# Performance work log

Measured on AMD Instinct MI355X. Metric: run time of the kernel, lower is better.

Reference implementation:

```python
import jax, jax.numpy as jnp
import numpy as np

N, E = 50000, 800000
IN_F, OUT_F, EMB, KER = 64, 64, 3, 4


def setup_inputs() -> dict:
    key = jax.random.key(0)
    ks = jax.random.split(key, 6)
    x = jax.random.normal(ks[0], (N, IN_F), dtype=jnp.float32)
    edge_idx = jax.random.randint(ks[1], (2, E), 0, N, dtype=jnp.int64)
    spec_domain = jax.random.normal(ks[2], (N, EMB), dtype=jnp.float32)
    weight = 0.1 * jax.random.normal(ks[3], (IN_F, OUT_F, KER), dtype=jnp.float32)
    bias_p = 0.1 * jax.random.normal(ks[4], (OUT_F,), dtype=jnp.float32)
    mu = 0.005 * jax.random.normal(ks[5], (EMB, KER), dtype=jnp.float32)
    sig = jnp.ones((1, KER), dtype=jnp.float32)  # repo default 60140 underflows exp with random embeddings
    return {"x": x, "edge_idx": edge_idx, "spec_domain": spec_domain,
            "weight": weight, "bias_p": bias_p, "mu": mu, "sig": sig}


def reference(x, edge_idx, spec_domain, weight, bias_p, mu, sig):
    n = x.shape[0]
    row, col = edge_idx[0], edge_idx[1]
    # support for all kernels at once: [N, out, K]
    support = jnp.einsum('ni,iok->nok', x, weight)
    # per-edge Gaussian kernel values: [E, K]
    diff = spec_domain[row] - spec_domain[col]               # [E, emb]
    dm = diff[:, :, None] - mu[None, :, :]                   # [E, emb, K]
    qq = -0.5 * jnp.sum(dm * dm, axis=1)                     # [E, K]
    value = jnp.exp(sig[0][None, :] * qq)                    # [E, K]
    # sparse mm: out[row] += value * support[col], per kernel
    msgs = value[:, None, :] * support[col]                  # [E, out, K]
    out = jax.ops.segment_sum(msgs, row, num_segments=n)     # [N, out, K]
    return out.sum(axis=2) + bias_p
```

## Files before the change

### kernel.cpp

```cpp
#include <hip/hip_runtime.h>
#include <hip/hip_fp16.h>

#define FIN 64
#define CAP 64
#define CSTR 16

__global__ __launch_bounds__(256) void prep_kernel(const int* __restrict__ eidx,
                                                   int* __restrict__ flag,
                                                   int4* __restrict__ cnt4, int n4) {
    int i = blockIdx.x * blockDim.x + threadIdx.x;
    if (i == 0) {
        int nz = 0;
        for (int j = 1; j < 16; j += 2) nz |= eidx[j];
        *flag = (nz == 0) ? 1 : 0;
    }
    int4 z = make_int4(0, 0, 0, 0);
    for (int t = i; t < n4; t += gridDim.x * blockDim.x) cnt4[t] = z;
}

__global__ __launch_bounds__(256) void mid_kernel(const float* __restrict__ x,
                                                  const float* __restrict__ weight,
                                                  __half* __restrict__ sup,
                                                  const int* __restrict__ eidx,
                                                  const int* __restrict__ flag,
                                                  int* __restrict__ cnt,
                                                  int* __restrict__ scol,
                                                  int n, int e_total) {
    const int t = threadIdx.x;

    __shared__ float xs[32][64];
    const int rowbase = blockIdx.x * 32;

    if (rowbase < n) {
        {
            const float4* __restrict__ x4 = (const float4*)(x + (size_t)rowbase * 64);
            float4* __restrict__ s4 = (float4*)&xs[0][0];
            int limit = (n - rowbase) * 16;
            if (limit > 512) limit = 512;
            #pragma unroll
            for (int j = 0; j < 2; ++j) {
                int idx = t + j * 256;
                if (idx < limit) s4[idx] = x4[idx];
            }
        }
        __syncthreads();

        const int w = t >> 6;
        const int o = t & 63;

        float4 acc[8];
        #pragma unroll
        for (int r = 0; r < 8; ++r) acc[r] = make_float4(0.f, 0.f, 0.f, 0.f);

        #pragma unroll 4
        for (int ic = 0; ic < 16; ++ic) {
            float4 w0 = *(const float4*)&weight[(ic * 4 + 0) * 256 + o * 4];
            float4 w1 = *(const float4*)&weight[(ic * 4 + 1) * 256 + o * 4];
            float4 w2 = *(const float4*)&weight[(ic * 4 + 2) * 256 + o * 4];
            float4 w3 = *(const float4*)&weight[(ic * 4 + 3) * 256 + o * 4];
            #pragma unroll
            for (int r = 0; r < 8; ++r) {
                float4 xv = *(const float4*)&xs[w * 8 + r][ic * 4];
                acc[r].x += xv.x * w0.x + xv.y * w1.x + xv.z * w2.x + xv.w * w3.x;
                acc[r].y += xv.x * w0.y + xv.y * w1.y + xv.z * w2.y + xv.w * w3.y;
                acc[r].z += xv.x * w0.z + xv.y * w1.z + xv.z * w2.z + xv.w * w3.z;
                acc[r].w += xv.x * w0.w + xv.y * w1.w + xv.z * w2.w + xv.w * w3.w;
            }
        }

        #pragma unroll
        for (int r = 0; r < 8; ++r) {
            int gr = rowbase + w * 8 + r;
            if (gr < n) {
                union { __half2 h[2]; uint2 u; } p;
                p.h[0] = __floats2half2_rn(acc[r].x, acc[r].y);
                p.h[1] = __floats2half2_rn(acc[r].z, acc[r].w);
                *(uint2*)&sup[(size_t)gr * 256 + o * 4] = p.u;
            }
        }
    }

    const int is64 = *flag;
    const int tid = blockIdx.x * blockDim.x + t;
    const int stride = gridDim.x * blockDim.x;
    const int pairs = (e_total + 1) >> 1;
    if (is64) {
        const int4* rows4 = (const int4*)eidx;
        const int4* cols4 = (const int4*)(eidx + 2 * (size_t)e_total);
        for (int p = tid; p < pairs; p += stride) {
            int4 rr = rows4[p];
            int4 cc = cols4[p];
            { int pos = atomicAdd(&cnt[rr.x * CSTR], 1); if (pos < CAP) scol[rr.x * CAP + pos] = cc.x; }
            if (2 * p + 1 < e_total) {
                int pos = atomicAdd(&cnt[rr.z * CSTR], 1); if (pos < CAP) scol[rr.z * CAP + pos] = cc.z;
            }
        }
    } else {
        const int2* rows2 = (const int2*)eidx;
        const int2* cols2 = (const int2*)(eidx + (size_t)e_total);
        for (int p = tid; p < pairs; p += stride) {
            int2 rr = rows2[p];
            int2 cc = cols2[p];
            { int pos = atomicAdd(&cnt[rr.x * CSTR], 1); if (pos < CAP) scol[rr.x * CAP + pos] = cc.x; }
            if (2 * p + 1 < e_total) {
                int pos = atomicAdd(&cnt[rr.y * CSTR], 1); if (pos < CAP) scol[rr.y * CAP + pos] = cc.y;
            }
        }
    }
}

__device__ __forceinline__ float dot_sup(uint2 p, float4 v) {
    float2 f0 = __half22float2(__builtin_bit_cast(__half2, p.x));
    float2 f1 = __half22float2(__builtin_bit_cast(__half2, p.y));
    return f0.x * v.x + f0.y * v.y + f1.x * v.z + f1.y * v.w;
}

__global__ __launch_bounds__(256, 6) void row_kernel(const int* __restrict__ cnt,
                                                     const int* __restrict__ scol,
                                                     const float* __restrict__ spec,
                                                     const float* __restrict__ mu,
                                                     const float* __restrict__ sig,
                                                     const __half* __restrict__ sup,
                                                     const float* __restrict__ bias,
                                                     float* __restrict__ out, int n) {
    __shared__ float vlds[4][64];
    const int lane = threadIdx.x & 63;
    const int wl = threadIdx.x >> 6;
    const int wv = __builtin_amdgcn_readfirstlane(blockIdx.x * 4 + wl);
    const int NW = gridDim.x * 4;

    const int k  = lane & 3;
    const int es = lane >> 2;
    const float mu0 = mu[k], mu1 = mu[4 + k], mu2 = mu[8 + k];
    const float sgk = sig[k];
    const float bias_l = bias[lane];
    const unsigned un = (unsigned)n;

    for (int r = wv; r < n; r += NW) {
        int ecount = cnt[r * CSTR];
        if (ecount > CAP) ecount = CAP;
        const int base = r * CAP;
        const float sr0 = spec[r * 3 + 0];
        const float sr1 = spec[r * 3 + 1];
        const float sr2 = spec[r * 3 + 2];
        float acc = bias_l;

        for (int j = 0; j < ecount; j += 16) {
            int nb = ecount - j; if (nb > 16) nb = 16;

            float myv = 0.f;
            if (es < nb) {
                int mycol = scol[base + j + es];
                float d0 = sr0 - spec[mycol * 3 + 0];
                float d1 = sr1 - spec[mycol * 3 + 1];
                float d2 = sr2 - spec[mycol * 3 + 2];
                float a = d0 - mu0, b = d1 - mu1, c = d2 - mu2;
                myv = __expf(sgk * (-0.5f * (a * a + b * b + c * c)));
            }
            vlds[wl][lane] = myv;

            int nbr = (nb + 7) & ~7;
            for (int ee = 0; ee < nbr; ee += 8) {
                int c0 = scol[base + j + ee + 0];
                int c1 = scol[base + j + ee + 1];
                int c2 = scol[base + j + ee + 2];
                int c3 = scol[base + j + ee + 3];
                int c4 = scol[base + j + ee + 4];
                int c5 = scol[base + j + ee + 5];
                int c6 = scol[base + j + ee + 6];
                int c7 = scol[base + j + ee + 7];
                c0 = ((unsigned)c0 < un) ? c0 : 0;
                c1 = ((unsigned)c1 < un) ? c1 : 0;
                c2 = ((unsigned)c2 < un) ? c2 : 0;
                c3 = ((unsigned)c3 < un) ? c3 : 0;
                c4 = ((unsigned)c4 < un) ? c4 : 0;
                c5 = ((unsigned)c5 < un) ? c5 : 0;
                c6 = ((unsigned)c6 < un) ? c6 : 0;
                c7 = ((unsigned)c7 < un) ? c7 : 0;
                uint2 p0 = *(const uint2*)(sup + ((size_t)c0 * 256 + lane * 4));
                uint2 p1 = *(const uint2*)(sup + ((size_t)c1 * 256 + lane * 4));
                uint2 p2 = *(const uint2*)(sup + ((size_t)c2 * 256 + lane * 4));
                uint2 p3 = *(const uint2*)(sup + ((size_t)c3 * 256 + lane * 4));
                uint2 p4 = *(const uint2*)(sup + ((size_t)c4 * 256 + lane * 4));
                uint2 p5 = *(const uint2*)(sup + ((size_t)c5 * 256 + lane * 4));
                uint2 p6 = *(const uint2*)(sup + ((size_t)c6 * 256 + lane * 4));
                uint2 p7 = *(const uint2*)(sup + ((size_t)c7 * 256 + lane * 4));
                float4 v0 = *(const float4*)&vlds[wl][(ee + 0) * 4];
                float4 v1 = *(const float4*)&vlds[wl][(ee + 1) * 4];
                float4 v2 = *(const float4*)&vlds[wl][(ee + 2) * 4];
                float4 v3 = *(const float4*)&vlds[wl][(ee + 3) * 4];
                float4 v4 = *(const float4*)&vlds[wl][(ee + 4) * 4];
                float4 v5 = *(const float4*)&vlds[wl][(ee + 5) * 4];
                float4 v6 = *(const float4*)&vlds[wl][(ee + 6) * 4];
                float4 v7 = *(const float4*)&vlds[wl][(ee + 7) * 4];
                acc += dot_sup(p0, v0);
                acc += dot_sup(p1, v1);
                acc += dot_sup(p2, v2);
                acc += dot_sup(p3, v3);
                acc += dot_sup(p4, v4);
                acc += dot_sup(p5, v5);
                acc += dot_sup(p6, v6);
                acc += dot_sup(p7, v7);
            }
        }
        out[(size_t)r * 64 + lane] = acc;
    }
}

extern "C" void kernel_launch(void* const* d_in, const int* in_sizes, int n_in,
                              void* d_out, int out_size, void* d_ws, size_t ws_size,
                              hipStream_t stream) {
    const float* x      = (const float*)d_in[0];
    const int*   eidx   = (const int*)d_in[1];
    const float* spec   = (const float*)d_in[2];
    const float* weight = (const float*)d_in[3];
    const float* bias   = (const float*)d_in[4];
    const float* mu     = (const float*)d_in[5];
    const float* sig    = (const float*)d_in[6];
    float* out = (float*)d_out;

    const int N = in_sizes[0] / FIN;
    const int E = in_sizes[1] / 2;

    char* w = (char*)d_ws;
    size_t off = 0;
    int* flag = (int*)(w + off);            off += 256;
    __half* sup = (__half*)(w + off);       off += (size_t)N * 256 * sizeof(__half);
    off = (off + 255) & ~(size_t)255;
    int* cnt = (int*)(w + off);             off += (size_t)N * CSTR * 4;
    off = (off + 255) & ~(size_t)255;
    int* scol = (int*)(w + off);            off += (size_t)N * CAP * 4;

    prep_kernel<<<2048, 256, 0, stream>>>(eidx, flag, (int4*)cnt, N * CSTR / 4);
    mid_kernel<<<(N + 31) / 32, 256, 0, stream>>>(x, weight, sup, eidx, flag, cnt, scol, N, E);
    row_kernel<<<1536, 256, 0, stream>>>(cnt, scol, spec, mu, sig, sup, bias, out, N);
}
```

Before: 126.5 us.

## Bucket edges by 32-row blocks with sliced counters and LDS atomic accumulation

Replaces the per-row CSR-like bucketing (one counter per row, padded stride) with per-32-row-block buckets split into 8 slices chosen by producer block, packing column and local row into one int. This shrinks the counter array and zeroing cost, and spreads global atomic contention across slices. The consumer now handles one 32-row block per workgroup, accumulating messages with shared-memory float atomics before writing output. The trade-off is LDS atomics on every message and a fixed 128-edge cap per slice; random imbalance could drop edges if a slice overflows.

```diff
diff --git a/kernel.cpp b/kernel.cpp
--- a/kernel.cpp
+++ b/kernel.cpp
@@ -2,20 +2,20 @@
 #include <hip/hip_fp16.h>
 
 #define FIN 64
-#define CAP 64
-#define CSTR 16
+#define BROWS 32
+#define NSLICE 8
+#define SCAP 128
 
 __global__ __launch_bounds__(256) void prep_kernel(const int* __restrict__ eidx,
                                                    int* __restrict__ flag,
-                                                   int4* __restrict__ cnt4, int n4) {
+                                                   int* __restrict__ cnt2, int total) {
     int i = blockIdx.x * blockDim.x + threadIdx.x;
     if (i == 0) {
         int nz = 0;
         for (int j = 1; j < 16; j += 2) nz |= eidx[j];
         *flag = (nz == 0) ? 1 : 0;
     }
-    int4 z = make_int4(0, 0, 0, 0);
-    for (int t = i; t < n4; t += gridDim.x * blockDim.x) cnt4[t] = z;
+    for (; i < total; i += gridDim.x * blockDim.x) cnt2[i] = 0;
 }
 
 __global__ __launch_bounds__(256) void mid_kernel(const float* __restrict__ x,
@@ -23,9 +23,9 @@
                                                   __half* __restrict__ sup,
                                                   const int* __restrict__ eidx,
                                                   const int* __restrict__ flag,
-                                                  int* __restrict__ cnt,
-                                                  int* __restrict__ scol,
-                                                  int n, int e_total) {
+                                                  int* __restrict__ cnt2,
+                                                  int* __restrict__ part,
+                                                  int n, int e_total, int nb1) {
     const int t = threadIdx.x;
 
     __shared__ float xs[32][64];
@@ -81,18 +81,27 @@
     }
 
     const int is64 = *flag;
+    const int s = blockIdx.x & (NSLICE - 1);
+    int* __restrict__ mycnt = cnt2 + s * nb1;
     const int tid = blockIdx.x * blockDim.x + t;
     const int stride = gridDim.x * blockDim.x;
     const int pairs = (e_total + 1) >> 1;
+
     if (is64) {
         const int4* rows4 = (const int4*)eidx;
         const int4* cols4 = (const int4*)(eidx + 2 * (size_t)e_total);
         for (int p = tid; p < pairs; p += stride) {
             int4 rr = rows4[p];
             int4 cc = cols4[p];
-            { int pos = atomicAdd(&cnt[rr.x * CSTR], 1); if (pos < CAP) scol[rr.x * CAP + pos] = cc.x; }
+            {
+                int b = rr.x >> 5;
+                int pos = atomicAdd(&mycnt[b], 1);
+                if (pos < SCAP) part[((b * NSLICE + s) << 7) + pos] = (cc.x << 5) | (rr.x & 31);
+            }
             if (2 * p + 1 < e_total) {
-                int pos = atomicAdd(&cnt[rr.z * CSTR], 1); if (pos < CAP) scol[rr.z * CAP + pos] = cc.z;
+                int b = rr.z >> 5;
+                int pos = atomicAdd(&mycnt[b], 1);
+                if (pos < SCAP) part[((b * NSLICE + s) << 7) + pos] = (cc.z << 5) | (rr.z & 31);
             }
         }
     } else {
@@ -101,9 +110,15 @@
         for (int p = tid; p < pairs; p += stride) {
             int2 rr = rows2[p];
             int2 cc = cols2[p];
-            { int pos = atomicAdd(&cnt[rr.x * CSTR], 1); if (pos < CAP) scol[rr.x * CAP + pos] = cc.x; }
+            {
+                int b = rr.x >> 5;
+                int pos = atomicAdd(&mycnt[b], 1);
+                if (pos < SCAP) part[((b * NSLICE + s) << 7) + pos] = (cc.x << 5) | (rr.x & 31);
+            }
             if (2 * p + 1 < e_total) {
-                int pos = atomicAdd(&cnt[rr.y * CSTR], 1); if (pos < CAP) scol[rr.y * CAP + pos] = cc.y;
+                int b = rr.y >> 5;
+                int pos = atomicAdd(&mycnt[b], 1);
+                if (pos < SCAP) part[((b * NSLICE + s) << 7) + pos] = (cc.y << 5) | (rr.y & 31);
             }
         }
     }
@@ -115,60 +130,70 @@
     return f0.x * v.x + f0.y * v.y + f1.x * v.z + f1.y * v.w;
 }
 
-__global__ __launch_bounds__(256, 6) void row_kernel(const int* __restrict__ cnt,
-                                                     const int* __restrict__ scol,
-                                                     const float* __restrict__ spec,
-                                                     const float* __restrict__ mu,
-                                                     const float* __restrict__ sig,
-                                                     const __half* __restrict__ sup,
-                                                     const float* __restrict__ bias,
-                                                     float* __restrict__ out, int n) {
+__global__ __launch_bounds__(256) void consume_kernel(const int* __restrict__ cnt2,
+                                                      const int* __restrict__ part,
+                                                      const float* __restrict__ spec,
+                                                      const float* __restrict__ mu,
+                                                      const float* __restrict__ sig,
+                                                      const __half* __restrict__ sup,
+                                                      const float* __restrict__ bias,
+                                                      float* __restrict__ out, int n, int nb1) {
+    __shared__ float accs[BROWS][64];
     __shared__ float vlds[4][64];
-    const int lane = threadIdx.x & 63;
-    const int wl = threadIdx.x >> 6;
-    const int wv = __builtin_amdgcn_readfirstlane(blockIdx.x * 4 + wl);
-    const int NW = gridDim.x * 4;
+    const int t = threadIdx.x;
+    const int lane = t & 63;
+    const int wl = t >> 6;
+    const int b = blockIdx.x;
+    const int row0 = b * BROWS;
+
+    {
+        float4* a4 = (float4*)&accs[0][0];
+        a4[t] = make_float4(0.f, 0.f, 0.f, 0.f);
+        a4[t + 256] = make_float4(0.f, 0.f, 0.f, 0.f);
+    }
+    __syncthreads();
 
     const int k  = lane & 3;
     const int es = lane >> 2;
     const float mu0 = mu[k], mu1 = mu[4 + k], mu2 = mu[8 + k];
     const float sgk = sig[k];
-    const float bias_l = bias[lane];
     const unsigned un = (unsigned)n;
 
-    for (int r = wv; r < n; r += NW) {
-        int ecount = cnt[r * CSTR];
-        if (ecount > CAP) ecount = CAP;
-        const int base = r * CAP;
-        const float sr0 = spec[r * 3 + 0];
-        const float sr1 = spec[r * 3 + 1];
-        const float sr2 = spec[r * 3 + 2];
-        float acc = bias_l;
-
-        for (int j = 0; j < ecount; j += 16) {
-            int nb = ecount - j; if (nb > 16) nb = 16;
+    #pragma unroll
+    for (int si = 0; si < 2; ++si) {
+        const int s = wl * 2 + si;
+        int ec = cnt2[s * nb1 + b];
+        if (ec > SCAP) ec = SCAP;
+        const int base = (b * NSLICE + s) << 7;
+
+        for (int j = 0; j < ec; j += 16) {
+            int nb = ec - j; if (nb > 16) nb = 16;
 
             float myv = 0.f;
             if (es < nb) {
-                int mycol = scol[base + j + es];
-                float d0 = sr0 - spec[mycol * 3 + 0];
-                float d1 = sr1 - spec[mycol * 3 + 1];
-                float d2 = sr2 - spec[mycol * 3 + 2];
-                float a = d0 - mu0, b = d1 - mu1, c = d2 - mu2;
-                myv = __expf(sgk * (-0.5f * (a * a + b * b + c * c)));
+                int pk = part[base + j + es];
+                int rl = pk & 31;
+                int mycol = pk >> 5;
+                float d0 = spec[(row0 + rl) * 3 + 0] - spec[mycol * 3 + 0];
+                float d1 = spec[(row0 + rl) * 3 + 1] - spec[mycol * 3 + 1];
+                float d2 = spec[(row0 + rl) * 3 + 2] - spec[mycol * 3 + 2];
+                float a = d0 - mu0, bb = d1 - mu1, c = d2 - mu2;
+                myv = __expf(sgk * (-0.5f * (a * a + bb * bb + c * c)));
             }
             vlds[wl][lane] = myv;
 
             int nbr = (nb + 7) & ~7;
             for (int ee = 0; ee < nbr; ee += 8) {
-                int c0 = scol[base + j + ee + 0];
-                int c1 = scol[base + j + ee + 1];
-                int c2 = scol[base + j + ee + 2];
-                int c3 = scol[base + j + ee + 3];
-                int c4 = scol[base + j + ee + 4];
-                int c5 = scol[base + j + ee + 5];
-                int c6 = scol[base + j + ee + 6];
-                int c7 = scol[base + j + ee + 7];
+                int pk0 = part[base + j + ee + 0];
+                int pk1 = part[base + j + ee + 1];
+                int pk2 = part[base + j + ee + 2];
+                int pk3 = part[base + j + ee + 3];
+                int pk4 = part[base + j + ee + 4];
+                int pk5 = part[base + j + ee + 5];
+                int pk6 = part[base + j + ee + 6];
+                int pk7 = part[base + j + ee + 7];
+                int c0 = pk0 >> 5, c1 = pk1 >> 5, c2 = pk2 >> 5, c3 = pk3 >> 5;
+                int c4 = pk4 >> 5, c5 = pk5 >> 5, c6 = pk6 >> 5, c7 = pk7 >> 5;
                 c0 = ((unsigned)c0 < un) ? c0 : 0;
                 c1 = ((unsigned)c1 < un) ? c1 : 0;
                 c2 = ((unsigned)c2 < un) ? c2 : 0;
@@ -193,17 +218,33 @@
                 float4 v5 = *(const float4*)&vlds[wl][(ee + 5) * 4];
                 float4 v6 = *(const float4*)&vlds[wl][(ee + 6) * 4];
                 float4 v7 = *(const float4*)&vlds[wl][(ee + 7) * 4];
-                acc += dot_sup(p0, v0);
-                acc += dot_sup(p1, v1);
-                acc += dot_sup(p2, v2);
-                acc += dot_sup(p3, v3);
-                acc += dot_sup(p4, v4);
-                acc += dot_sup(p5, v5);
-                acc += dot_sup(p6, v6);
-                acc += dot_sup(p7, v7);
-            }
-        }
-        out[(size_t)r * 64 + lane] = acc;
+                float m0 = dot_sup(p0, v0);
+                float m1 = dot_sup(p1, v1);
+                float m2 = dot_sup(p2, v2);
+                float m3 = dot_sup(p3, v3);
+                float m4 = dot_sup(p4, v4);
+                float m5 = dot_sup(p5, v5);
+                float m6 = dot_sup(p6, v6);
+                float m7 = dot_sup(p7, v7);
+                atomicAdd(&accs[pk0 & 31][lane], m0);
+                atomicAdd(&accs[pk1 & 31][lane], m1);
+                atomicAdd(&accs[pk2 & 31][lane], m2);
+                atomicAdd(&accs[pk3 & 31][lane], m3);
+                atomicAdd(&accs[pk4 & 31][lane], m4);
+                atomicAdd(&accs[pk5 & 31][lane], m5);
+                atomicAdd(&accs[pk6 & 31][lane], m6);
+                atomicAdd(&accs[pk7 & 31][lane], m7);
+            }
+        }
+    }
+    __syncthreads();
+
+    #pragma unroll
+    for (int j = 0; j < 8; ++j) {
+        int idx = t + j * 256;
+        int r = idx >> 6, c = idx & 63;
+        int row = row0 + r;
+        if (row < n) out[(size_t)row * 64 + c] = accs[r][c] + bias[c];
     }
 }
 
@@ -221,17 +262,18 @@
 
     const int N = in_sizes[0] / FIN;
     const int E = in_sizes[1] / 2;
+    const int NB1 = (N + BROWS - 1) / BROWS;
 
     char* w = (char*)d_ws;
     size_t off = 0;
     int* flag = (int*)(w + off);            off += 256;
     __half* sup = (__half*)(w + off);       off += (size_t)N * 256 * sizeof(__half);
     off = (off + 255) & ~(size_t)255;
-    int* cnt = (int*)(w + off);             off += (size_t)N * CSTR * 4;
+    int* cnt2 = (int*)(w + off);            off += (size_t)NSLICE * NB1 * 4;
     off = (off + 255) & ~(size_t)255;
-    int* scol = (int*)(w + off);            off += (size_t)N * CAP * 4;
-
-    prep_kernel<<<2048, 256, 0, stream>>>(eidx, flag, (int4*)cnt, N * CSTR / 4);
-    mid_kernel<<<(N + 31) / 32, 256, 0, stream>>>(x, weight, sup, eidx, flag, cnt, scol, N, E);
-    row_kernel<<<1536, 256, 0, stream>>>(cnt, scol, spec, mu, sig, sup, bias, out, N);
-}
+    int* part = (int*)(w + off);            off += (size_t)NB1 * NSLICE * SCAP * 4;
+
+    prep_kernel<<<64, 256, 0, stream>>>(eidx, flag, cnt2, NSLICE * NB1);
+    mid_kernel<<<NB1, 256, 0, stream>>>(x, weight, sup, eidx, flag, cnt2, part, N, E, NB1);
+    consume_kernel<<<NB1, 256, 0, stream>>>(cnt2, part, spec, mu, sig, sup, bias, out, N, NB1);
+}
```

Result: slower. 386.0 us (+205.1%).
